# Kernel optimization log

Measured on AMD Instinct MI355X. Metric: run time of the kernel, lower is better.

## Reference

```python
import jax, jax.numpy as jnp
import numpy as np

EMB = 128
HID = 128
N = 1024


def setup_inputs() -> dict:
    key = jax.random.key(0)
    ks = jax.random.split(key, 10)
    s1 = 1.0 / np.sqrt(2 * EMB)
    s2 = 1.0 / np.sqrt(HID)
    return {
        "z1": jax.random.normal(ks[0], (N, EMB), jnp.float32),
        "z2": jax.random.normal(ks[1], (N, EMB), jnp.float32),
        "W1": jax.random.uniform(ks[2], (HID, 2 * EMB), jnp.float32, -s1, s1),
        "b1": jax.random.uniform(ks[3], (HID,), jnp.float32, -s1, s1),
        "W2": jax.random.uniform(ks[4], (HID, HID), jnp.float32, -s2, s2),
        "b2": jax.random.uniform(ks[5], (HID,), jnp.float32, -s2, s2),
        "W3": jax.random.uniform(ks[6], (1, HID), jnp.float32, -s2, s2),
        "b3": jax.random.uniform(ks[7], (1,), jnp.float32, -s2, s2),
    }


def reference(z1, z2, W1, b1, W2, b2, W3, b3):
    # pairs[i, j] = concat(z1[j], z2[i]); first Linear split into two matmuls
    # so the [n, n, 2*emb] concat tensor is never materialized (same math).
    W1a = W1[:, :EMB]   # acts on z1 half
    W1b = W1[:, EMB:]   # acts on z2 half
    a = jnp.einsum('jd,hd->jh', z1, W1a)          # [n, h], varies along j
    b = jnp.einsum('id,hd->ih', z2, W1b)          # [n, h], varies along i
    h1 = jax.nn.gelu(a[None, :, :] + b[:, None, :] + b1, approximate=False)  # [n, n, h]
    h2 = jax.nn.gelu(jnp.einsum('ijh,gh->ijg', h1, W2) + b2, approximate=False)
    log_q = jnp.einsum('ijh,oh->ijo', h2, W3) + b3  # [n, n, 1]
    return log_q[..., 0]
```

## Files before the change

kernel.cpp:

```cpp
#include <hip/hip_runtime.h>

#define NN  1024
#define EMB 128
#define HID 128

typedef __attribute__((ext_vector_type(4))) float float4v;
typedef __attribute__((ext_vector_type(8))) short short8;

__device__ __forceinline__ float gelu_fast(float x) {
  float x2 = x * x;
  float t = __builtin_fmaf(0.1029432f, x2, 2.3022086f);
  float e = __builtin_amdgcn_exp2f(x * t);
  float r = __builtin_amdgcn_rcpf(1.0f + e);
  return __builtin_fmaf(-x, r, x);
}

__global__ void prep_kernel(const float* __restrict__ z1, const float* __restrict__ z2,
                            const float* __restrict__ W1, const float* __restrict__ b1,
                            const float* __restrict__ W2,
                            float* __restrict__ Abuf, float* __restrict__ Bbuf,
                            unsigned short* __restrict__ W2f) {
  int blk = blockIdx.x;
  int tid = threadIdx.x;
  if (blk < 2 * NN) {
    int which = blk >> 10;
    int row = blk & (NN - 1);
    const float* z = which ? z2 : z1;
    __shared__ __align__(16) float zs[EMB];
    zs[tid] = z[row * EMB + tid];
    __syncthreads();
    const float4v* wrow = (const float4v*)(W1 + tid * (2 * EMB) + which * EMB);
    const float4v* zv = (const float4v*)zs;
    float acc = which ? 0.0f : b1[tid];
#pragma unroll
    for (int d = 0; d < EMB / 4; ++d) {
      float4v wv = wrow[d];
      float4v zz = zv[d];
      acc += zz[0] * wv[0] + zz[1] * wv[1] + zz[2] * wv[2] + zz[3] * wv[3];
    }
    (which ? Bbuf : Abuf)[row * HID + tid] = acc;
  } else {
    int idx = (blk - 2 * NN) * 1024 + tid * 8;
    int lane = (idx >> 3) & 63;
    int nt = (idx >> 9) & 7;
    int kt = idx >> 12;
    int g = nt * 16 + (lane & 15);
    int hb = kt * 32 + (lane >> 4) * 8;
#pragma unroll
    for (int j = 0; j < 8; ++j) {
      unsigned u = __float_as_uint(W2[g * HID + hb + j]);
      W2f[idx + j] = (unsigned short)((u + 0x7FFFu + ((u >> 16) & 1u)) >> 16);
    }
  }
}

__global__ __launch_bounds__(256, 2)
void fused_mlp_kernel(const float* __restrict__ Abuf, const float* __restrict__ Bbuf,
                      const float* __restrict__ W2f4,
                      const float* __restrict__ b2, const float* __restrict__ W3,
                      const float* __restrict__ b3, float* __restrict__ out) {
  __shared__ __align__(16) short s_w2[HID * HID];

  int tid = threadIdx.x;
  {
    const float4v* src = (const float4v*)W2f4;
    float4v* dst = (float4v*)s_w2;
#pragma unroll
    for (int t = 0; t < 8; ++t)
      dst[tid + t * 256] = src[tid + t * 256];
  }

  int w = tid >> 6;
  int l = tid & 63;
  int r = l & 15;
  int q = l >> 4;

  int bi = (blockIdx.x >> 6) << 4;
  int bj = (blockIdx.x & 63) << 4;

  const float* Arow = Abuf + (bj + r) * HID;
  const float* Bbase = Bbuf + (bi + (w << 2)) * HID;

  float4v acc[4][8] = {};

  __syncthreads();

#pragma unroll
  for (int kt = 0; kt < 4; ++kt) {
    int h0 = kt * 32 + q * 8;
    float4v a0 = *(const float4v*)(Arow + h0);
    float4v a1 = *(const float4v*)(Arow + h0 + 4);
    short8 bfr[8];
#pragma unroll
    for (int nt = 0; nt < 8; ++nt)
      bfr[nt] = ((const short8*)s_w2)[(kt * 8 + nt) * 64 + l];
#pragma unroll
    for (int mt = 0; mt < 4; ++mt) {
      const float* Brow = Bbase + mt * HID + h0;
      float4v c0 = *(const float4v*)(Brow);
      float4v c1 = *(const float4v*)(Brow + 4);
      short8 af;
#pragma unroll
      for (int j = 0; j < 4; ++j) {
        float g0 = gelu_fast(a0[j] + c0[j]);
        float g1 = gelu_fast(a1[j] + c1[j]);
        af[j]     = (short)((__float_as_uint(g0) + 0x8000u) >> 16);
        af[j + 4] = (short)((__float_as_uint(g1) + 0x8000u) >> 16);
      }
#pragma unroll
      for (int nt = 0; nt < 8; ++nt)
        acc[mt][nt] = __builtin_amdgcn_mfma_f32_16x16x32_bf16(af, bfr[nt], acc[mt][nt], 0, 0, 0);
    }
  }

  float b2v[8], w3v[8];
#pragma unroll
  for (int nt = 0; nt < 8; ++nt) {
    b2v[nt] = b2[nt * 16 + r];
    w3v[nt] = W3[nt * 16 + r];
  }
  float bias3 = b3[0];

#pragma unroll
  for (int mt = 0; mt < 4; ++mt) {
    float4v s = {0.f, 0.f, 0.f, 0.f};
#pragma unroll
    for (int nt = 0; nt < 8; ++nt) {
      float4v x = acc[mt][nt];
#pragma unroll
      for (int reg = 0; reg < 4; ++reg)
        s[reg] = __builtin_fmaf(gelu_fast(x[reg] + b2v[nt]), w3v[nt], s[reg]);
    }
#pragma unroll
    for (int mask = 1; mask < 16; mask <<= 1) {
#pragma unroll
      for (int reg = 0; reg < 4; ++reg)
        s[reg] += __shfl_xor(s[reg], mask, 64);
    }
    if (r < 4) {
      int irow = bi + (w << 2) + mt;
      int jcol = bj + q * 4 + r;
      out[irow * NN + jcol] = s[r] + bias3;
    }
  }
}

extern "C" void kernel_launch(void* const* d_in, const int* in_sizes, int n_in,
                              void* d_out, int out_size, void* d_ws, size_t ws_size,
                              hipStream_t stream) {
  const float* z1 = (const float*)d_in[0];
  const float* z2 = (const float*)d_in[1];
  const float* W1 = (const float*)d_in[2];
  const float* b1 = (const float*)d_in[3];
  const float* W2 = (const float*)d_in[4];
  const float* b2 = (const float*)d_in[5];
  const float* W3 = (const float*)d_in[6];
  const float* b3 = (const float*)d_in[7];
  float* out = (float*)d_out;

  float* Abuf = (float*)d_ws;
  float* Bbuf = Abuf + NN * HID;
  unsigned short* W2f = (unsigned short*)(Bbuf + NN * HID);

  prep_kernel<<<2 * NN + 16, 128, 0, stream>>>(z1, z2, W1, b1, W2, Abuf, Bbuf, W2f);
  fused_mlp_kernel<<<(NN / 16) * (NN / 16), 256, 0, stream>>>(
      Abuf, Bbuf, (const float*)W2f, b2, W3, b3, out);
}
```

Measured before the change: 185.4 us.

## Shrink fused MLP tile to 8x16 pairs, raise occupancy, MFMA-based prep

```diff
diff --git a/kernel.cpp b/kernel.cpp
--- a/kernel.cpp
+++ b/kernel.cpp
@@ -7,40 +7,77 @@
 typedef __attribute__((ext_vector_type(4))) float float4v;
 typedef __attribute__((ext_vector_type(8))) short short8;
 
-__device__ __forceinline__ float gelu_fast(float x) {
-  float x2 = x * x;
-  float t = __builtin_fmaf(0.1029432f, x2, 2.3022086f);
-  float e = __builtin_amdgcn_exp2f(x * t);
-  float r = __builtin_amdgcn_rcpf(1.0f + e);
-  return __builtin_fmaf(-x, r, x);
-}
-
-__global__ void prep_kernel(const float* __restrict__ z1, const float* __restrict__ z2,
-                            const float* __restrict__ W1, const float* __restrict__ b1,
-                            const float* __restrict__ W2,
-                            float* __restrict__ Abuf, float* __restrict__ Bbuf,
-                            unsigned short* __restrict__ W2f) {
+__device__ __forceinline__ float4v gelu4(float4v x) {
+  float4v x2 = x * x;
+  float4v t = x2 * 0.1029432f + 2.3022086f;
+  float4v y = x * t;
+  float4v e;
+  e[0] = __builtin_amdgcn_exp2f(y[0]);
+  e[1] = __builtin_amdgcn_exp2f(y[1]);
+  e[2] = __builtin_amdgcn_exp2f(y[2]);
+  e[3] = __builtin_amdgcn_exp2f(y[3]);
+  float4v d = e + 1.0f;
+  float4v rv;
+  rv[0] = __builtin_amdgcn_rcpf(d[0]);
+  rv[1] = __builtin_amdgcn_rcpf(d[1]);
+  rv[2] = __builtin_amdgcn_rcpf(d[2]);
+  rv[3] = __builtin_amdgcn_rcpf(d[3]);
+  return x - x * rv;
+}
+
+__device__ __forceinline__ short bfrh(float g) {
+  return (short)((__float_as_uint(g) + 0x8000u) >> 16);
+}
+
+__global__ __launch_bounds__(256)
+void prep_kernel(const float* __restrict__ z1, const float* __restrict__ z2,
+                 const float* __restrict__ W1, const float* __restrict__ b1,
+                 const float* __restrict__ W2,
+                 float* __restrict__ Abuf, float* __restrict__ Bbuf,
+                 unsigned short* __restrict__ W2f) {
   int blk = blockIdx.x;
   int tid = threadIdx.x;
-  if (blk < 2 * NN) {
-    int which = blk >> 10;
-    int row = blk & (NN - 1);
+  if (blk < 128) {
+    int which = blk >> 6;
+    int j0 = (blk & 63) << 4;
     const float* z = which ? z2 : z1;
-    __shared__ __align__(16) float zs[EMB];
-    zs[tid] = z[row * EMB + tid];
-    __syncthreads();
-    const float4v* wrow = (const float4v*)(W1 + tid * (2 * EMB) + which * EMB);
-    const float4v* zv = (const float4v*)zs;
-    float acc = which ? 0.0f : b1[tid];
-#pragma unroll
-    for (int d = 0; d < EMB / 4; ++d) {
-      float4v wv = wrow[d];
-      float4v zz = zv[d];
-      acc += zz[0] * wv[0] + zz[1] * wv[1] + zz[2] * wv[2] + zz[3] * wv[3];
-    }
-    (which ? Bbuf : Abuf)[row * HID + tid] = acc;
+    int w = tid >> 6, l = tid & 63, r = l & 15, q = l >> 4;
+
+    const float* zrow = z + (j0 + r) * EMB;
+    const float* w1r0 = W1 + (w * 32 + r) * (2 * EMB) + which * EMB;
+    const float* w1r1 = w1r0 + 16 * (2 * EMB);
+
+    float4v acc[2] = {};
+#pragma unroll
+    for (int kt = 0; kt < 4; ++kt) {
+      int k0 = kt * 32 + q * 8;
+      float4v za = *(const float4v*)(zrow + k0);
+      float4v zb = *(const float4v*)(zrow + k0 + 4);
+      float4v wa0 = *(const float4v*)(w1r0 + k0);
+      float4v wb0 = *(const float4v*)(w1r0 + k0 + 4);
+      float4v wa1 = *(const float4v*)(w1r1 + k0);
+      float4v wb1 = *(const float4v*)(w1r1 + k0 + 4);
+      short8 az, b0f, b1f;
+#pragma unroll
+      for (int j = 0; j < 4; ++j) {
+        az[j] = bfrh(za[j]);  az[j + 4] = bfrh(zb[j]);
+        b0f[j] = bfrh(wa0[j]); b0f[j + 4] = bfrh(wb0[j]);
+        b1f[j] = bfrh(wa1[j]); b1f[j + 4] = bfrh(wb1[j]);
+      }
+      acc[0] = __builtin_amdgcn_mfma_f32_16x16x32_bf16(az, b0f, acc[0], 0, 0, 0);
+      acc[1] = __builtin_amdgcn_mfma_f32_16x16x32_bf16(az, b1f, acc[1], 0, 0, 0);
+    }
+    float ba0 = which ? 0.0f : b1[w * 32 + r];
+    float ba1 = which ? 0.0f : b1[w * 32 + 16 + r];
+    float* dst = which ? Bbuf : Abuf;
+#pragma unroll
+    for (int reg = 0; reg < 4; ++reg) {
+      int row = j0 + q * 4 + reg;
+      dst[row * HID + w * 32 + r]      = acc[0][reg] + ba0;
+      dst[row * HID + w * 32 + 16 + r] = acc[1][reg] + ba1;
+    }
   } else {
-    int idx = (blk - 2 * NN) * 1024 + tid * 8;
+    int idx = (blk - 128) * 2048 + tid * 8;
     int lane = (idx >> 3) & 63;
     int nt = (idx >> 9) & 7;
     int kt = idx >> 12;
@@ -54,7 +91,7 @@
   }
 }
 
-__global__ __launch_bounds__(256, 2)
+__global__ __launch_bounds__(256, 4)
 void fused_mlp_kernel(const float* __restrict__ Abuf, const float* __restrict__ Bbuf,
                       const float* __restrict__ W2f4,
                       const float* __restrict__ b2, const float* __restrict__ W3,
@@ -75,13 +112,14 @@
   int r = l & 15;
   int q = l >> 4;
 
-  int bi = (blockIdx.x >> 6) << 4;
+  int bi = (blockIdx.x >> 6) << 3;
   int bj = (blockIdx.x & 63) << 4;
 
   const float* Arow = Abuf + (bj + r) * HID;
-  const float* Bbase = Bbuf + (bi + (w << 2)) * HID;
-
-  float4v acc[4][8] = {};
+  const float* B0 = Bbuf + (bi + w * 2) * HID;
+  const float* B1 = B0 + HID;
+
+  float4v acc[2][8] = {};
 
   __syncthreads();
 
@@ -90,26 +128,24 @@
     int h0 = kt * 32 + q * 8;
     float4v a0 = *(const float4v*)(Arow + h0);
     float4v a1 = *(const float4v*)(Arow + h0 + 4);
-    short8 bfr[8];
-#pragma unroll
-    for (int nt = 0; nt < 8; ++nt)
-      bfr[nt] = ((const short8*)s_w2)[(kt * 8 + nt) * 64 + l];
-#pragma unroll
-    for (int mt = 0; mt < 4; ++mt) {
-      const float* Brow = Bbase + mt * HID + h0;
-      float4v c0 = *(const float4v*)(Brow);
-      float4v c1 = *(const float4v*)(Brow + 4);
-      short8 af;
-#pragma unroll
-      for (int j = 0; j < 4; ++j) {
-        float g0 = gelu_fast(a0[j] + c0[j]);
-        float g1 = gelu_fast(a1[j] + c1[j]);
-        af[j]     = (short)((__float_as_uint(g0) + 0x8000u) >> 16);
-        af[j + 4] = (short)((__float_as_uint(g1) + 0x8000u) >> 16);
-      }
-#pragma unroll
-      for (int nt = 0; nt < 8; ++nt)
-        acc[mt][nt] = __builtin_amdgcn_mfma_f32_16x16x32_bf16(af, bfr[nt], acc[mt][nt], 0, 0, 0);
+
+    float4v g00 = gelu4(a0 + *(const float4v*)(B0 + h0));
+    float4v g01 = gelu4(a1 + *(const float4v*)(B0 + h0 + 4));
+    float4v g10 = gelu4(a0 + *(const float4v*)(B1 + h0));
+    float4v g11 = gelu4(a1 + *(const float4v*)(B1 + h0 + 4));
+    short8 af0, af1;
+#pragma unroll
+    for (int j = 0; j < 4; ++j) {
+      af0[j] = bfrh(g00[j]); af0[j + 4] = bfrh(g01[j]);
+      af1[j] = bfrh(g10[j]); af1[j + 4] = bfrh(g11[j]);
+    }
+
+    const short8* wrow = (const short8*)s_w2 + kt * 8 * 64 + l;
+#pragma unroll
+    for (int nt = 0; nt < 8; ++nt) {
+      short8 bfr = wrow[nt * 64];
+      acc[0][nt] = __builtin_amdgcn_mfma_f32_16x16x32_bf16(af0, bfr, acc[0][nt], 0, 0, 0);
+      acc[1][nt] = __builtin_amdgcn_mfma_f32_16x16x32_bf16(af1, bfr, acc[1][nt], 0, 0, 0);
     }
   }
 
@@ -122,14 +158,12 @@
   float bias3 = b3[0];
 
 #pragma unroll
-  for (int mt = 0; mt < 4; ++mt) {
+  for (int mt = 0; mt < 2; ++mt) {
     float4v s = {0.f, 0.f, 0.f, 0.f};
 #pragma unroll
     for (int nt = 0; nt < 8; ++nt) {
-      float4v x = acc[mt][nt];
-#pragma unroll
-      for (int reg = 0; reg < 4; ++reg)
-        s[reg] = __builtin_fmaf(gelu_fast(x[reg] + b2v[nt]), w3v[nt], s[reg]);
+      float4v xx = acc[mt][nt] + b2v[nt];
+      s = s + gelu4(xx) * w3v[nt];
     }
 #pragma unroll
     for (int mask = 1; mask < 16; mask <<= 1) {
@@ -138,7 +172,7 @@
         s[reg] += __shfl_xor(s[reg], mask, 64);
     }
     if (r < 4) {
-      int irow = bi + (w << 2) + mt;
+      int irow = bi + w * 2 + mt;
       int jcol = bj + q * 4 + r;
       out[irow * NN + jcol] = s[r] + bias3;
     }
@@ -162,7 +196,7 @@
   float* Bbuf = Abuf + NN * HID;
   unsigned short* W2f = (unsigned short*)(Bbuf + NN * HID);
 
-  prep_kernel<<<2 * NN + 16, 128, 0, stream>>>(z1, z2, W1, b1, W2, Abuf, Bbuf, W2f);
-  fused_mlp_kernel<<<(NN / 16) * (NN / 16), 256, 0, stream>>>(
+  prep_kernel<<<136, 256, 0, stream>>>(z1, z2, W1, b1, W2, Abuf, Bbuf, W2f);
+  fused_mlp_kernel<<<(NN / 8) * (NN / 16), 256, 0, stream>>>(
       Abuf, Bbuf, (const float*)W2f, b2, W3, b3, out);
 }
```

Result: faster. 159.5 us (-14.0%).
